# Optimization experiments

Hardware: AMD Instinct MI355X
Metric: run time of the kernel (lower is better)

## Reference

```python
import jax, jax.numpy as jnp
import numpy as np

B, K, C, NCLS = 256, 32, 2048, 20
EPS = 1e-4
MARGIN = 150.0
TRIP_MARGIN = 0.8
T = 0.07


def setup_inputs() -> dict:
    key = jax.random.key(0)
    ks = jax.random.split(key, 8)
    video_scores = jax.random.uniform(ks[0], (B, NCLS), jnp.float32, EPS, 1.0 - EPS)
    label = (jax.random.uniform(ks[1], (B, NCLS)) < 0.15).astype(jnp.float32)
    # guarantee every video has at least one positive class (avoids div-by-zero in label norm)
    fix = jax.nn.one_hot(jax.random.randint(ks[2], (B,), 0, NCLS), NCLS, dtype=jnp.float32)
    label = jnp.where((label.sum(axis=1, keepdims=True) > 0), label, fix)
    PA = jax.random.normal(ks[3], (B, K, C), jnp.float32)
    PB = jax.random.normal(ks[4], (B, K, C), jnp.float32)
    NA = jax.random.normal(ks[5], (B, K, C), jnp.float32)
    NB = jax.random.normal(ks[6], (B, K, C), jnp.float32)
    return {"video_scores": video_scores, "label": label, "PA": PA, "PB": PB, "NA": NA, "NB": NB}


def _nce(q, k, neg):
    # q,k: [B,C]; neg: [B,K,C] -> permuted to [B,C,K], normalized over C
    q = q / jnp.linalg.norm(q, axis=1, keepdims=True)
    k = k / jnp.linalg.norm(k, axis=1, keepdims=True)
    negp = jnp.transpose(neg, (0, 2, 1))  # [B,C,K]
    negp = negp / jnp.linalg.norm(negp, axis=1, keepdims=True)
    l_pos = jnp.einsum('nc,nc->n', q, k)[:, None]        # [B,1]
    l_neg = jnp.einsum('nc,nck->nk', q, negp)            # [B,K]
    logits = jnp.concatenate([l_pos, l_neg], axis=1) / T
    # CE with target class 0
    return -jax.nn.log_softmax(logits, axis=1)[:, 0].mean()


def _triplet(label, PA):
    n = label.shape[0]
    act = PA.mean(axis=2)  # [B,K] -- original averages over channels per snippet
    an = act / jnp.linalg.norm(act, axis=1, keepdims=True)
    D = 1.0 - an @ an.T    # [B,B] pairwise cosine distance
    idxs = jnp.arange(n)

    def per_class(m):  # m: bool [B] membership of this class
        cnt = m.sum()
        # anchor = last element of the Python set iteration = max member index
        anchor = jnp.max(jnp.where(m, idxs, -1))
        row = D[anchor]
        others = idxs != anchor
        max_d = jnp.maximum(0.0, jnp.max(jnp.where(m & others, row, -jnp.inf)))
        min_d = jnp.minimum(jnp.max(row), jnp.min(jnp.where(~m, row, jnp.inf)))
        contrib = jnp.maximum(max_d - min_d + TRIP_MARGIN, 0.0)
        return jnp.where(cnt > 1, contrib, 0.0)

    masks = (label == 1).T  # [NCLS, B]
    return jax.vmap(per_class)(masks).sum()


def reference(video_scores, label, PA, PB, NA, NB):
    # Action (BCE) loss with row-normalized labels
    lbl = label / label.sum(axis=1, keepdims=True)
    p = video_scores
    loss_cls = -(lbl * jnp.log(p) + (1.0 - lbl) * jnp.log(1.0 - p)).mean()

    # SniCo NCE
    loss_snico = _nce(NA.mean(axis=1), PA.mean(axis=1), PB) + _nce(NB.mean(axis=1), PB.mean(axis=1), PA)

    # Abs (uncertainty-margin) loss
    la = jnp.maximum(MARGIN - jnp.linalg.norm(PA.mean(axis=1), axis=1), 0.0)
    lb = jnp.linalg.norm(PB.mean(axis=1), axis=1)
    loss_abs = jnp.mean((la + lb) ** 2)

    # Triplet loss (vectorized version of the serial mining)
    loss_triplet = _triplet(label, PA)

    loss_total = loss_cls + 0.01 * loss_snico + 0.0005 * loss_abs + 0.005 * loss_triplet
    return (loss_total, loss_cls, loss_snico, loss_abs, loss_triplet)
```

## Files before the change

kernel.cpp:

```cpp
#include <hip/hip_runtime.h>
#include <math.h>

#define BATCH 256
#define KSNIP 32
#define CH    2048
#define CH4   512
#define NCLSS 20

#define OFF_MNA 0
#define OFF_MNB 524288
#define OFF_PK  1048576
#define PKN 8192
#define OFF_SC  1089536

__device__ __forceinline__ float dot4(float4 a, float4 b) {
    return a.x*b.x + a.y*b.y + a.z*b.z + a.w*b.w;
}
__device__ __forceinline__ float sum4(float4 a) { return a.x + a.y + a.z + a.w; }
__device__ __forceinline__ float4 add4(float4 a, float4 b) {
    return make_float4(a.x+b.x, a.y+b.y, a.z+b.z, a.w+b.w);
}

__global__ __launch_bounds__(512) void meanNK_kernel(
    const float* __restrict__ NAp, const float* __restrict__ NBp,
    float* __restrict__ ws)
{
    const int t   = blockIdx.x >> 8;
    const int b   = blockIdx.x & 255;
    const int tid = threadIdx.x;
    const int w   = tid >> 6;
    const int l   = tid & 63;

    const float4* src = (const float4*)((t ? NBp : NAp) + (size_t)b * KSNIP * CH);

    float4 cs[8];
    #pragma unroll
    for (int j = 0; j < 8; ++j) cs[j] = make_float4(0.f,0.f,0.f,0.f);

    #pragma unroll
    for (int kk = 0; kk < 4; ++kk) {
        const int k = w + kk*8;
        float4 v[8];
        #pragma unroll
        for (int j = 0; j < 8; ++j) v[j] = src[k*CH4 + l + j*64];
        #pragma unroll
        for (int j = 0; j < 8; ++j) cs[j] = add4(cs[j], v[j]);
    }

    __shared__ float4 sCol[CH4];
    __shared__ float  sW[8];
    for (int wv = 0; wv < 8; ++wv) {
        if (w == wv) {
            #pragma unroll
            for (int j = 0; j < 8; ++j) {
                const int c = l + j*64;
                sCol[c] = (wv == 0) ? cs[j] : add4(sCol[c], cs[j]);
            }
        }
        __syncthreads();
    }

    float4 m = sCol[tid];
    const float s = 1.0f/32.0f;
    m.x *= s; m.y *= s; m.z *= s; m.w *= s;
    ((float4*)(ws + (t ? OFF_MNB : OFF_MNA) + b*CH))[tid] = m;

    float v2 = dot4(m, m);
    #pragma unroll
    for (int o = 32; o; o >>= 1) v2 += __shfl_xor(v2, o);
    if (l == 0) sW[w] = v2;
    __syncthreads();
    if (tid == 0) {
        float tot = 0.f;
        #pragma unroll
        for (int i = 0; i < 8; ++i) tot += sW[i];
        ws[OFF_SC + (2 + t)*256 + b] = tot;
    }
}

__global__ __launch_bounds__(512) void dots_kernel(
    const float* __restrict__ PA, const float* __restrict__ PB,
    float* __restrict__ ws)
{
    const int t   = blockIdx.x >> 8;
    const int b   = blockIdx.x & 255;
    const int tid = threadIdx.x;
    const int w   = tid >> 6;
    const int l   = tid & 63;

    const float4* src  = (const float4*)((t ? PB : PA) + (size_t)b * KSNIP * CH);
    const float4* mDot = (const float4*)(ws + (t ? OFF_MNA : OFF_MNB) + b*CH);
    const float4* mDap = (const float4*)(ws + (t ? OFF_MNB : OFF_MNA) + b*CH);

    float4 md[8];
    #pragma unroll
    for (int j = 0; j < 8; ++j) md[j] = mDot[l + j*64];

    float4 cs[8];
    #pragma unroll
    for (int j = 0; j < 8; ++j) cs[j] = make_float4(0.f,0.f,0.f,0.f);

    float dqA[4], sqA[4], rsA[4];

    #pragma unroll
    for (int kk = 0; kk < 4; ++kk) {
        const int k = w + kk*8;
        float4 v[8];
        #pragma unroll
        for (int j = 0; j < 8; ++j) v[j] = src[k*CH4 + l + j*64];

        float dq = 0.f, sq = 0.f, rs = 0.f;
        #pragma unroll
        for (int j = 0; j < 8; ++j) {
            cs[j] = add4(cs[j], v[j]);
            dq += dot4(md[j], v[j]);
            sq += dot4(v[j], v[j]);
            rs += sum4(v[j]);
        }
        dqA[kk] = dq; sqA[kk] = sq; rsA[kk] = rs;
    }

    #pragma unroll
    for (int kk = 0; kk < 4; ++kk) {
        #pragma unroll
        for (int o = 32; o; o >>= 1) {
            dqA[kk] += __shfl_xor(dqA[kk], o);
            sqA[kk] += __shfl_xor(sqA[kk], o);
            rsA[kk] += __shfl_xor(rsA[kk], o);
        }
        if (l == 0) {
            const int idx = (w + kk*8)*BATCH + b;
            if (t == 0) {
                ws[OFF_PK + 2*PKN + idx] = dqA[kk];
                ws[OFF_PK + 3*PKN + idx] = sqA[kk];
                ws[OFF_PK + 4*PKN + idx] = rsA[kk];
            } else {
                ws[OFF_PK + 0*PKN + idx] = dqA[kk];
                ws[OFF_PK + 1*PKN + idx] = sqA[kk];
            }
        }
    }

    __shared__ float4 sCol[CH4];
    __shared__ float  sW[8][2];
    for (int wv = 0; wv < 8; ++wv) {
        if (w == wv) {
            #pragma unroll
            for (int j = 0; j < 8; ++j) {
                const int c = l + j*64;
                sCol[c] = (wv == 0) ? cs[j] : add4(sCol[c], cs[j]);
            }
        }
        __syncthreads();
    }

    float4 m = sCol[tid];
    const float s = 1.0f/32.0f;
    m.x *= s; m.y *= s; m.z *= s; m.w *= s;
    float n2  = dot4(m, m);
    float dap = dot4(mDap[tid], m);
    #pragma unroll
    for (int o = 32; o; o >>= 1) {
        n2  += __shfl_xor(n2, o);
        dap += __shfl_xor(dap, o);
    }
    if (l == 0) { sW[w][0] = n2; sW[w][1] = dap; }
    __syncthreads();
    if (tid == 0) {
        float t0 = 0.f, t1 = 0.f;
        #pragma unroll
        for (int i = 0; i < 8; ++i) { t0 += sW[i][0]; t1 += sW[i][1]; }
        ws[OFF_SC + t*256 + b]       = t0;
        ws[OFF_SC + (4 + t)*256 + b] = t1;
    }
}

__global__ __launch_bounds__(256) void finish_kernel(
    const float* __restrict__ vs, const float* __restrict__ label,
    const float* __restrict__ ws, float* __restrict__ out)
{
    const int tid  = threadIdx.x;
    const int b    = tid;
    const int lane = tid & 63;
    const int w    = tid >> 6;

    __shared__ float sLab[NCLSS*BATCH];
    __shared__ float sVS [NCLSS*BATCH];
    __shared__ float an[BATCH][33];
    __shared__ float sD[NCLSS][BATCH];
    __shared__ unsigned long long sMask[NCLSS][4];
    __shared__ int   sAnchor[NCLSS];
    __shared__ int   sCnt[NCLSS];
    __shared__ float sbuf[4];
    __shared__ float stp[4];

    const float* pk = ws + OFF_PK;

    #pragma unroll
    for (int j = 0; j < NCLSS; ++j) {
        const int i = j*BATCH + tid;
        const int c = i % NCLSS;
        const int bb = i / NCLSS;
        sLab[c*BATCH + bb] = label[i];
        sVS [c*BATCH + bb] = vs[i];
    }
    #pragma unroll
    for (int j = 0; j < KSNIP; ++j) {
        const int i = j*BATCH + tid;
        an[i & 255][i >> 8] = pk[4*PKN + i];
    }
    __syncthreads();

    {
        float nrm = 0.f;
        #pragma unroll
        for (int k = 0; k < KSNIP; ++k) { float v = an[b][k]; nrm += v*v; }
        const float inv = 1.0f / sqrtf(nrm);
        #pragma unroll
        for (int k = 0; k < KSNIP; ++k) an[b][k] *= inv;
    }

    const float invT = 1.0f / 0.07f;
    const float nPA = sqrtf(ws[OFF_SC + 0*256 + b]);
    const float nPB = sqrtf(ws[OFF_SC + 1*256 + b]);
    const float nNA = sqrtf(ws[OFF_SC + 2*256 + b]);
    const float nNB = sqrtf(ws[OFF_SC + 3*256 + b]);
    const float dAP = ws[OFF_SC + 4*256 + b];
    const float dBP = ws[OFF_SC + 5*256 + b];

    float nce;
    {
        const float lpos = dAP / (nNA * nPA) * invT;
        float vv[KSNIP];
        #pragma unroll
        for (int k = 0; k < KSNIP; ++k) {
            const float dq = pk[0*PKN + k*BATCH + b];
            const float sq = pk[1*PKN + k*BATCH + b];
            vv[k] = dq * invT / (nNA * sqrtf(sq));
        }
        float m = lpos;
        #pragma unroll
        for (int k = 0; k < KSNIP; ++k) m = fmaxf(m, vv[k]);
        float s = expf(lpos - m);
        #pragma unroll
        for (int k = 0; k < KSNIP; ++k) s += expf(vv[k] - m);
        nce = logf(s) + m - lpos;
    }
    {
        const float lpos = dBP / (nNB * nPB) * invT;
        float vv[KSNIP];
        #pragma unroll
        for (int k = 0; k < KSNIP; ++k) {
            const float dq = pk[2*PKN + k*BATCH + b];
            const float sq = pk[3*PKN + k*BATCH + b];
            vv[k] = dq * invT / (nNB * sqrtf(sq));
        }
        float m = lpos;
        #pragma unroll
        for (int k = 0; k < KSNIP; ++k) m = fmaxf(m, vv[k]);
        float s = expf(lpos - m);
        #pragma unroll
        for (int k = 0; k < KSNIP; ++k) s += expf(vv[k] - m);
        nce += logf(s) + m - lpos;
    }

    const float la   = fmaxf(150.0f - nPA, 0.0f);
    const float absb = (la + nPB) * (la + nPB);

    float rs = 0.0f;
    #pragma unroll
    for (int c = 0; c < NCLSS; ++c) rs += sLab[c*BATCH + b];
    float clsb = 0.0f;
    #pragma unroll
    for (int c = 0; c < NCLSS; ++c) {
        const float l = sLab[c*BATCH + b] / rs;
        const float p = sVS [c*BATCH + b];
        clsb -= l * logf(p) + (1.0f - l) * logf(1.0f - p);
    }

    auto blocksum = [&](float v) -> float {
        #pragma unroll
        for (int o = 32; o; o >>= 1) v += __shfl_xor(v, o);
        __syncthreads();
        if (lane == 0) sbuf[w] = v;
        __syncthreads();
        return sbuf[0] + sbuf[1] + sbuf[2] + sbuf[3];
    };

    const float loss_snico = blocksum(nce)  / 256.0f;
    const float loss_abs   = blocksum(absb) / 256.0f;
    const float loss_cls   = blocksum(clsb) / 5120.0f;

    #pragma unroll
    for (int c = 0; c < NCLSS; ++c) {
        const bool mm = sLab[c*BATCH + b] > 0.5f;
        const unsigned long long mk = __ballot(mm);
        if (lane == 0) sMask[c][w] = mk;
    }
    __syncthreads();
    if (tid < NCLSS) {
        int cnt = 0, anchor = -1;
        #pragma unroll
        for (int q = 3; q >= 0; --q) {
            const unsigned long long mq = sMask[tid][q];
            cnt += __builtin_popcountll(mq);
            if (anchor < 0 && mq) anchor = q*64 + 63 - __builtin_clzll(mq);
        }
        sAnchor[tid] = anchor;
        sCnt[tid]    = cnt;
    }
    __syncthreads();

    #pragma unroll
    for (int c = 0; c < NCLSS; ++c) {
        if (sCnt[c] > 1) {
            const int a = sAnchor[c];
            float acc = 0.f;
            #pragma unroll
            for (int k = 0; k < KSNIP; ++k) acc += an[a][k] * an[b][k];
            sD[c][b] = 1.0f - acc;
        }
    }
    __syncthreads();

    float tripw = 0.f;
    #pragma unroll
    for (int cc = 0; cc < 5; ++cc) {
        const int c = w*5 + cc;
        if (sCnt[c] > 1) {
            const int a = sAnchor[c];
            float vAll = -__builtin_inff();
            float vMem = -__builtin_inff();
            float vNon =  __builtin_inff();
            #pragma unroll
            for (int q = 0; q < 4; ++q) {
                const int bb = lane + q*64;
                const float d = sD[c][bb];
                const bool mm = (sMask[c][q] >> lane) & 1ull;
                vAll = fmaxf(vAll, d);
                if (mm && bb != a) vMem = fmaxf(vMem, d);
                if (!mm)           vNon = fminf(vNon, d);
            }
            #pragma unroll
            for (int o = 32; o; o >>= 1) {
                vAll = fmaxf(vAll, __shfl_xor(vAll, o));
                vMem = fmaxf(vMem, __shfl_xor(vMem, o));
                vNon = fminf(vNon, __shfl_xor(vNon, o));
            }
            if (lane == 0) {
                const float max_d = fmaxf(0.0f, vMem);
                const float min_d = fminf(vAll, vNon);
                tripw += fmaxf(max_d - min_d + 0.8f, 0.0f);
            }
        }
    }
    if (lane == 0) stp[w] = tripw;
    __syncthreads();

    if (tid == 0) {
        const float trip_total = stp[0] + stp[1] + stp[2] + stp[3];
        const float total = loss_cls + 0.01f * loss_snico + 0.0005f * loss_abs + 0.005f * trip_total;
        out[0] = total;
        out[1] = loss_cls;
        out[2] = loss_snico;
        out[3] = loss_abs;
        out[4] = trip_total;
    }
}

extern "C" void kernel_launch(void* const* d_in, const int* in_sizes, int n_in,
                              void* d_out, int out_size, void* d_ws, size_t ws_size,
                              hipStream_t stream) {
    const float* vs    = (const float*)d_in[0];
    const float* label = (const float*)d_in[1];
    const float* PA    = (const float*)d_in[2];
    const float* PB    = (const float*)d_in[3];
    const float* NAp   = (const float*)d_in[4];
    const float* NBp   = (const float*)d_in[5];
    float* ws  = (float*)d_ws;
    float* out = (float*)d_out;

    meanNK_kernel<<<dim3(512), dim3(512), 0, stream>>>(NAp, NBp, ws);
    dots_kernel  <<<dim3(512), dim3(512), 0, stream>>>(PA, PB, ws);
    finish_kernel<<<dim3(1),   dim3(256), 0, stream>>>(vs, label, ws, out);
}
```

Before: 89.67 us.

## Split channels across wave pairs and double-buffer snippet row loads

After: 85.44 us. 4.7% less time.

```diff
diff --git a/kernel.cpp b/kernel.cpp
--- a/kernel.cpp
+++ b/kernel.cpp
@@ -30,31 +30,39 @@
     const int tid = threadIdx.x;
     const int w   = tid >> 6;
     const int l   = tid & 63;
+    const int ch  = (w & 1)*256 + l;
+    const int kr  = w >> 1;
 
     const float4* src = (const float4*)((t ? NBp : NAp) + (size_t)b * KSNIP * CH);
 
-    float4 cs[8];
-    #pragma unroll
-    for (int j = 0; j < 8; ++j) cs[j] = make_float4(0.f,0.f,0.f,0.f);
-
-    #pragma unroll
-    for (int kk = 0; kk < 4; ++kk) {
-        const int k = w + kk*8;
-        float4 v[8];
-        #pragma unroll
-        for (int j = 0; j < 8; ++j) v[j] = src[k*CH4 + l + j*64];
-        #pragma unroll
-        for (int j = 0; j < 8; ++j) cs[j] = add4(cs[j], v[j]);
+    float4 cs[4];
+    #pragma unroll
+    for (int j = 0; j < 4; ++j) cs[j] = make_float4(0.f,0.f,0.f,0.f);
+
+    float4 v[2][4];
+    #pragma unroll
+    for (int j = 0; j < 4; ++j) v[0][j] = src[kr*CH4 + ch + j*64];
+
+    #pragma unroll
+    for (int kk = 0; kk < 8; ++kk) {
+        if (kk < 7) {
+            const int kn = kr + (kk+1)*4;
+            #pragma unroll
+            for (int j = 0; j < 4; ++j) v[(kk+1)&1][j] = src[kn*CH4 + ch + j*64];
+        }
+        #pragma unroll
+        for (int j = 0; j < 4; ++j) cs[j] = add4(cs[j], v[kk&1][j]);
     }
 
     __shared__ float4 sCol[CH4];
     __shared__ float  sW[8];
-    for (int wv = 0; wv < 8; ++wv) {
-        if (w == wv) {
-            #pragma unroll
-            for (int j = 0; j < 8; ++j) {
-                const int c = l + j*64;
-                sCol[c] = (wv == 0) ? cs[j] : add4(sCol[c], cs[j]);
+    #pragma unroll
+    for (int p = 0; p < 4; ++p) {
+        if ((w >> 1) == p) {
+            #pragma unroll
+            for (int j = 0; j < 4; ++j) {
+                const int c = ch + j*64;
+                sCol[c] = (p == 0) ? cs[j] : add4(sCol[c], cs[j]);
             }
         }
         __syncthreads();
@@ -87,41 +95,49 @@
     const int tid = threadIdx.x;
     const int w   = tid >> 6;
     const int l   = tid & 63;
+    const int ch  = (w & 1)*256 + l;
+    const int kr  = w >> 1;
 
     const float4* src  = (const float4*)((t ? PB : PA) + (size_t)b * KSNIP * CH);
     const float4* mDot = (const float4*)(ws + (t ? OFF_MNA : OFF_MNB) + b*CH);
     const float4* mDap = (const float4*)(ws + (t ? OFF_MNB : OFF_MNA) + b*CH);
 
-    float4 md[8];
-    #pragma unroll
-    for (int j = 0; j < 8; ++j) md[j] = mDot[l + j*64];
-
-    float4 cs[8];
-    #pragma unroll
-    for (int j = 0; j < 8; ++j) cs[j] = make_float4(0.f,0.f,0.f,0.f);
-
-    float dqA[4], sqA[4], rsA[4];
-
-    #pragma unroll
-    for (int kk = 0; kk < 4; ++kk) {
-        const int k = w + kk*8;
-        float4 v[8];
-        #pragma unroll
-        for (int j = 0; j < 8; ++j) v[j] = src[k*CH4 + l + j*64];
-
+    float4 md[4];
+    #pragma unroll
+    for (int j = 0; j < 4; ++j) md[j] = mDot[ch + j*64];
+
+    float4 cs[4];
+    #pragma unroll
+    for (int j = 0; j < 4; ++j) cs[j] = make_float4(0.f,0.f,0.f,0.f);
+
+    float dqA[8], sqA[8], rsA[8];
+
+    float4 v[2][4];
+    #pragma unroll
+    for (int j = 0; j < 4; ++j) v[0][j] = src[kr*CH4 + ch + j*64];
+
+    #pragma unroll
+    for (int kk = 0; kk < 8; ++kk) {
+        if (kk < 7) {
+            const int kn = kr + (kk+1)*4;
+            #pragma unroll
+            for (int j = 0; j < 4; ++j) v[(kk+1)&1][j] = src[kn*CH4 + ch + j*64];
+        }
         float dq = 0.f, sq = 0.f, rs = 0.f;
         #pragma unroll
-        for (int j = 0; j < 8; ++j) {
-            cs[j] = add4(cs[j], v[j]);
-            dq += dot4(md[j], v[j]);
-            sq += dot4(v[j], v[j]);
-            rs += sum4(v[j]);
+        for (int j = 0; j < 4; ++j) {
+            const float4 vv = v[kk&1][j];
+            cs[j] = add4(cs[j], vv);
+            dq += dot4(md[j], vv);
+            sq += dot4(vv, vv);
+            rs += sum4(vv);
         }
         dqA[kk] = dq; sqA[kk] = sq; rsA[kk] = rs;
     }
 
-    #pragma unroll
-    for (int kk = 0; kk < 4; ++kk) {
+    __shared__ float sPar[8][8][3];
+    #pragma unroll
+    for (int kk = 0; kk < 8; ++kk) {
         #pragma unroll
         for (int o = 32; o; o >>= 1) {
             dqA[kk] += __shfl_xor(dqA[kk], o);
@@ -129,26 +145,40 @@
             rsA[kk] += __shfl_xor(rsA[kk], o);
         }
         if (l == 0) {
-            const int idx = (w + kk*8)*BATCH + b;
-            if (t == 0) {
-                ws[OFF_PK + 2*PKN + idx] = dqA[kk];
-                ws[OFF_PK + 3*PKN + idx] = sqA[kk];
-                ws[OFF_PK + 4*PKN + idx] = rsA[kk];
-            } else {
-                ws[OFF_PK + 0*PKN + idx] = dqA[kk];
-                ws[OFF_PK + 1*PKN + idx] = sqA[kk];
-            }
+            sPar[w][kk][0] = dqA[kk];
+            sPar[w][kk][1] = sqA[kk];
+            sPar[w][kk][2] = rsA[kk];
+        }
+    }
+    __syncthreads();
+
+    if (tid < KSNIP) {
+        const int k  = tid;
+        const int wp = 2*(k & 3);
+        const int kk = k >> 2;
+        const float dq = sPar[wp][kk][0] + sPar[wp+1][kk][0];
+        const float sq = sPar[wp][kk][1] + sPar[wp+1][kk][1];
+        const float rs = sPar[wp][kk][2] + sPar[wp+1][kk][2];
+        const int idx = k*BATCH + b;
+        if (t == 0) {
+            ws[OFF_PK + 2*PKN + idx] = dq;
+            ws[OFF_PK + 3*PKN + idx] = sq;
+            ws[OFF_PK + 4*PKN + idx] = rs;
+        } else {
+            ws[OFF_PK + 0*PKN + idx] = dq;
+            ws[OFF_PK + 1*PKN + idx] = sq;
         }
     }
 
     __shared__ float4 sCol[CH4];
     __shared__ float  sW[8][2];
-    for (int wv = 0; wv < 8; ++wv) {
-        if (w == wv) {
-            #pragma unroll
-            for (int j = 0; j < 8; ++j) {
-                const int c = l + j*64;
-                sCol[c] = (wv == 0) ? cs[j] : add4(sCol[c], cs[j]);
+    #pragma unroll
+    for (int p = 0; p < 4; ++p) {
+        if ((w >> 1) == p) {
+            #pragma unroll
+            for (int j = 0; j < 4; ++j) {
+                const int c = ch + j*64;
+                sCol[c] = (p == 0) ? cs[j] : add4(sCol[c], cs[j]);
             }
         }
         __syncthreads();
```

## Stage snippet rows via direct global-to-LDS loads with double buffering

Applied to the files above, without the earlier changes.

Measured after the change: 90.68 us. No clear change (+1.1%).

```diff
diff --git a/kernel.cpp b/kernel.cpp
--- a/kernel.cpp
+++ b/kernel.cpp
@@ -19,6 +19,17 @@
 __device__ __forceinline__ float sum4(float4 a) { return a.x + a.y + a.z + a.w; }
 __device__ __forceinline__ float4 add4(float4 a, float4 b) {
     return make_float4(a.x+b.x, a.y+b.y, a.z+b.z, a.w+b.w);
+}
+
+__device__ __forceinline__ void gload_lds16(const float* g, float* l) {
+    __builtin_amdgcn_global_load_lds(
+        (const __attribute__((address_space(1))) void*)g,
+        (__attribute__((address_space(3))) void*)l,
+        16, 0, 0);
+}
+__device__ __forceinline__ void wait_vm0() {
+    asm volatile("s_waitcnt vmcnt(0)" ::: "memory");
+    __builtin_amdgcn_sched_barrier(0);
 }
 
 __global__ __launch_bounds__(512) void meanNK_kernel(
@@ -31,29 +42,42 @@
     const int w   = tid >> 6;
     const int l   = tid & 63;
 
-    const float4* src = (const float4*)((t ? NBp : NAp) + (size_t)b * KSNIP * CH);
-
-    float4 cs[8];
-    #pragma unroll
-    for (int j = 0; j < 8; ++j) cs[j] = make_float4(0.f,0.f,0.f,0.f);
-
-    #pragma unroll
-    for (int kk = 0; kk < 4; ++kk) {
-        const int k = w + kk*8;
-        float4 v[8];
-        #pragma unroll
-        for (int j = 0; j < 8; ++j) v[j] = src[k*CH4 + l + j*64];
-        #pragma unroll
-        for (int j = 0; j < 8; ++j) cs[j] = add4(cs[j], v[j]);
-    }
-
+    __shared__ float  sStage[8][2][CH];
     __shared__ float4 sCol[CH4];
     __shared__ float  sW[8];
+
+    const float* src = (t ? NBp : NAp) + (size_t)b * KSNIP * CH;
+    float* st0 = &sStage[w][0][0];
+    float* st1 = &sStage[w][1][0];
+
+    auto issue = [&](int k, float* dst) {
+        const float* rp = src + (size_t)k * CH + l * 4;
+        #pragma unroll
+        for (int j = 0; j < 8; ++j) gload_lds16(rp + j * 256, dst + j * 256);
+    };
+
+    float4 cs[8];
+    #pragma unroll
+    for (int j = 0; j < 8; ++j) cs[j] = make_float4(0.f, 0.f, 0.f, 0.f);
+
+    issue(w, st0);
+    wait_vm0();
+    #pragma unroll
+    for (int kk = 0; kk < 4; ++kk) {
+        float* cur = (kk & 1) ? st1 : st0;
+        float* nxt = (kk & 1) ? st0 : st1;
+        if (kk < 3) issue(w + (kk + 1) * 8, nxt);
+        const float4* c4 = (const float4*)cur;
+        #pragma unroll
+        for (int j = 0; j < 8; ++j) cs[j] = add4(cs[j], c4[j * 64 + l]);
+        wait_vm0();
+    }
+
     for (int wv = 0; wv < 8; ++wv) {
         if (w == wv) {
             #pragma unroll
             for (int j = 0; j < 8; ++j) {
-                const int c = l + j*64;
+                const int c = j * 64 + l;
                 sCol[c] = (wv == 0) ? cs[j] : add4(sCol[c], cs[j]);
             }
         }
@@ -61,9 +85,9 @@
     }
 
     float4 m = sCol[tid];
-    const float s = 1.0f/32.0f;
+    const float s = 1.0f / 32.0f;
     m.x *= s; m.y *= s; m.z *= s; m.w *= s;
-    ((float4*)(ws + (t ? OFF_MNB : OFF_MNA) + b*CH))[tid] = m;
+    ((float4*)(ws + (t ? OFF_MNB : OFF_MNA) + b * CH))[tid] = m;
 
     float v2 = dot4(m, m);
     #pragma unroll
@@ -74,7 +98,7 @@
         float tot = 0.f;
         #pragma unroll
         for (int i = 0; i < 8; ++i) tot += sW[i];
-        ws[OFF_SC + (2 + t)*256 + b] = tot;
+        ws[OFF_SC + (2 + t) * 256 + b] = tot;
     }
 }
 
@@ -88,36 +112,51 @@
     const int w   = tid >> 6;
     const int l   = tid & 63;
 
-    const float4* src  = (const float4*)((t ? PB : PA) + (size_t)b * KSNIP * CH);
-    const float4* mDot = (const float4*)(ws + (t ? OFF_MNA : OFF_MNB) + b*CH);
-    const float4* mDap = (const float4*)(ws + (t ? OFF_MNB : OFF_MNA) + b*CH);
+    __shared__ float  sStage[8][2][CH];
+    __shared__ float4 sCol[CH4];
+    __shared__ float  sW[8][2];
+
+    const float* src = (t ? PB : PA) + (size_t)b * KSNIP * CH;
+    const float4* mDot = (const float4*)(ws + (t ? OFF_MNA : OFF_MNB) + b * CH);
+    const float4* mDap = (const float4*)(ws + (t ? OFF_MNB : OFF_MNA) + b * CH);
+    float* st0 = &sStage[w][0][0];
+    float* st1 = &sStage[w][1][0];
+
+    auto issue = [&](int k, float* dst) {
+        const float* rp = src + (size_t)k * CH + l * 4;
+        #pragma unroll
+        for (int j = 0; j < 8; ++j) gload_lds16(rp + j * 256, dst + j * 256);
+    };
 
     float4 md[8];
     #pragma unroll
-    for (int j = 0; j < 8; ++j) md[j] = mDot[l + j*64];
+    for (int j = 0; j < 8; ++j) md[j] = mDot[j * 64 + l];
 
     float4 cs[8];
     #pragma unroll
-    for (int j = 0; j < 8; ++j) cs[j] = make_float4(0.f,0.f,0.f,0.f);
+    for (int j = 0; j < 8; ++j) cs[j] = make_float4(0.f, 0.f, 0.f, 0.f);
 
     float dqA[4], sqA[4], rsA[4];
 
+    issue(w, st0);
+    wait_vm0();
     #pragma unroll
     for (int kk = 0; kk < 4; ++kk) {
-        const int k = w + kk*8;
-        float4 v[8];
-        #pragma unroll
-        for (int j = 0; j < 8; ++j) v[j] = src[k*CH4 + l + j*64];
-
+        float* cur = (kk & 1) ? st1 : st0;
+        float* nxt = (kk & 1) ? st0 : st1;
+        if (kk < 3) issue(w + (kk + 1) * 8, nxt);
+        const float4* c4 = (const float4*)cur;
         float dq = 0.f, sq = 0.f, rs = 0.f;
         #pragma unroll
         for (int j = 0; j < 8; ++j) {
-            cs[j] = add4(cs[j], v[j]);
-            dq += dot4(md[j], v[j]);
-            sq += dot4(v[j], v[j]);
-            rs += sum4(v[j]);
+            const float4 a = c4[j * 64 + l];
+            cs[j] = add4(cs[j], a);
+            dq += dot4(md[j], a);
+            sq += dot4(a, a);
+            rs += sum4(a);
         }
         dqA[kk] = dq; sqA[kk] = sq; rsA[kk] = rs;
+        wait_vm0();
     }
 
     #pragma unroll
@@ -129,25 +168,24 @@
             rsA[kk] += __shfl_xor(rsA[kk], o);
         }
         if (l == 0) {
-            const int idx = (w + kk*8)*BATCH + b;
+            const int k   = w + kk * 8;
+            const int idx = k * BATCH + b;
             if (t == 0) {
-                ws[OFF_PK + 2*PKN + idx] = dqA[kk];
-                ws[OFF_PK + 3*PKN + idx] = sqA[kk];
-                ws[OFF_PK + 4*PKN + idx] = rsA[kk];
+                ws[OFF_PK + 2 * PKN + idx] = dqA[kk];
+                ws[OFF_PK + 3 * PKN + idx] = sqA[kk];
+                ws[OFF_PK + 4 * PKN + idx] = rsA[kk];
             } else {
-                ws[OFF_PK + 0*PKN + idx] = dqA[kk];
-                ws[OFF_PK + 1*PKN + idx] = sqA[kk];
-            }
-        }
-    }
-
-    __shared__ float4 sCol[CH4];
-    __shared__ float  sW[8][2];
+                ws[OFF_PK + 0 * PKN + idx] = dqA[kk];
+                ws[OFF_PK + 1 * PKN + idx] = sqA[kk];
+            }
+        }
+    }
+
     for (int wv = 0; wv < 8; ++wv) {
         if (w == wv) {
             #pragma unroll
             for (int j = 0; j < 8; ++j) {
-                const int c = l + j*64;
+                const int c = j * 64 + l;
                 sCol[c] = (wv == 0) ? cs[j] : add4(sCol[c], cs[j]);
             }
         }
@@ -155,7 +193,7 @@
     }
 
     float4 m = sCol[tid];
-    const float s = 1.0f/32.0f;
+    const float s = 1.0f / 32.0f;
     m.x *= s; m.y *= s; m.z *= s; m.w *= s;
     float n2  = dot4(m, m);
     float dap = dot4(mDap[tid], m);
@@ -170,8 +208,8 @@
         float t0 = 0.f, t1 = 0.f;
         #pragma unroll
         for (int i = 0; i < 8; ++i) { t0 += sW[i][0]; t1 += sW[i][1]; }
-        ws[OFF_SC + t*256 + b]       = t0;
-        ws[OFF_SC + (4 + t)*256 + b] = t1;
+        ws[OFF_SC + t * 256 + b]       = t0;
+        ws[OFF_SC + (4 + t) * 256 + b] = t1;
     }
 }
 
```
